# Kernel optimization log

Measured on AMD Instinct MI355X. Metric: run time of the kernel, lower is better.

The kernel has to match this reference:

```python
import jax, jax.numpy as jnp
import numpy as np

EPS = 1e-12
ALPHA = 0.5


def mlp(x, W1, b1, W2, b2):
    # 2-layer MLP (dropout inactive in eval mode) + row-wise l2 norm * 10
    h = jax.nn.relu(x @ W1 + b1)
    y = h @ W2 + b2
    n = jnp.maximum(jnp.linalg.norm(y, axis=-1, keepdims=True), EPS)
    return y / n * 10.0


def setup_inputs() -> dict:
    key = jax.random.key(0)
    ks = jax.random.split(key, 12)
    T, N, F = 3, 100000, 128
    M, E = 4, 65536
    B, H, O = 65536, 128, 64
    X = jax.random.normal(ks[0], (T, N, F), dtype=jnp.float32)
    s_features = jax.random.normal(ks[1], (B, F), dtype=jnp.float32)
    features_map = jax.random.randint(ks[2], (T, N), 0, N)
    s_idxs = jax.random.randint(ks[3], (M, T, E), 0, B)
    t_idxs = jax.random.randint(ks[4], (M, T, E), 0, N)
    weightss = jax.random.uniform(ks[5], (M, T, E), dtype=jnp.float32)
    W1 = jax.random.normal(ks[6], (F, H), dtype=jnp.float32) / np.sqrt(F)
    b1 = jnp.zeros((H,), dtype=jnp.float32)
    W2 = jax.random.normal(ks[7], (H, O), dtype=jnp.float32) / np.sqrt(H)
    b2 = jnp.zeros((O,), dtype=jnp.float32)
    metapath_weights = jnp.ones((M,), dtype=jnp.float32)
    ntype_weights = jnp.ones((T,), dtype=jnp.float32)
    return {"X": X, "s_features": s_features, "features_map": features_map,
            "s_idxs": s_idxs, "t_idxs": t_idxs, "weightss": weightss,
            "batch_size": B, "W1": W1, "b1": b1, "W2": W2, "b2": b2,
            "metapath_weights": metapath_weights, "ntype_weights": ntype_weights}


def reference(X, s_features, features_map, s_idxs, t_idxs, weightss,
              batch_size, W1, b1, W2, b2, metapath_weights, ntype_weights):
    M, T, E = s_idxs.shape
    O = W2.shape[1]
    nm = jax.nn.softmax(metapath_weights)  # [M]
    nt = jax.nn.softmax(ntype_weights)     # [T]
    t_arr = jnp.arange(T)[None, :, None]   # [1,T,1]
    map_idx = features_map[t_arr, t_idxs]  # [M,T,E]
    feats = X[t_arr, map_idx]              # [M,T,E,F] gather
    y = mlp(feats, W1, b1, W2, b2)         # [M,T,E,O]
    # fold metapath & type weights into per-edge weights (scatter is linear)
    ew = weightss * nt[None, :, None] * nm[:, None, None]  # [M,T,E]
    contrib = (y * ew[..., None]).reshape(-1, O)
    seg = s_idxs.reshape(-1)
    out = jax.ops.segment_sum(contrib, seg, num_segments=batch_size)  # [B,O]
    out = (1.0 - ALPHA) * out + ALPHA * mlp(s_features, W1, b1, W2, b2)
    return jax.nn.log_softmax(out, axis=1)
```

## Files before the change

### kernel.cpp

```cpp
#include <hip/hip_runtime.h>

#define Fdim 128
#define Hdim 128
#define Odim 64
#define RT 64
#define ECAP 64
#define EPSV 1e-12f
#define ALPHAV 0.5f

typedef _Float16 h8_t __attribute__((ext_vector_type(8)));
typedef _Float16 h4_t __attribute__((ext_vector_type(4)));
typedef float f32x4 __attribute__((ext_vector_type(4)));

#define X_OFF   0
#define H_OFF   16384
#define LDS_BYTES 32768
#define WIMG_BYTES 49152

extern "C" __global__ __launch_bounds__(512, 4)
void mlp_all(const float* __restrict__ X, const float* __restrict__ S,
             const char* __restrict__ wimg, const float* __restrict__ b1,
             const float* __restrict__ b2,
             _Float16* __restrict__ Yh, float* __restrict__ out,
             int TN, int rows_total)
{
    extern __shared__ char smem[];
    const int tid  = threadIdx.x;
    const int wave = tid >> 6;
    const int lane = tid & 63;
    const int c = lane & 15;
    const int g = lane >> 4;
    const int row0 = blockIdx.x * RT;

    h8_t w1f[4];
    #pragma unroll
    for (int kt = 0; kt < 4; ++kt)
        w1f[kt] = *(const h8_t*)(wimg + (((wave * 4 + kt) * 64 + lane) << 4));

    const int hbase = wave * 16 + 4 * g;
    float b1v[4];
    #pragma unroll
    for (int j = 0; j < 4; ++j) b1v[j] = b1[hbase + j];

    #pragma unroll
    for (int it = 0; it < 4; ++it) {
        int idx = tid + it * 512;
        int r = idx >> 5, c4 = idx & 31;
        int rowg = row0 + r;
        float4 v = make_float4(0.f, 0.f, 0.f, 0.f);
        if (rowg < TN)               v = *(const float4*)(X + (size_t)rowg * Fdim + c4 * 4);
        else if (rowg < rows_total)  v = *(const float4*)(S + (size_t)(rowg - TN) * Fdim + c4 * 4);
        h4_t hv;
        hv[0] = (_Float16)v.x; hv[1] = (_Float16)v.y;
        hv[2] = (_Float16)v.z; hv[3] = (_Float16)v.w;
        *(h4_t*)(smem + X_OFF + ((r * 256 + c4 * 8) ^ ((r & 7) << 4))) = hv;
    }
    __syncthreads();

    f32x4 acc[4];
    #pragma unroll
    for (int r = 0; r < 4; ++r) acc[r] = (f32x4){0.f, 0.f, 0.f, 0.f};

    #pragma unroll
    for (int kt = 0; kt < 4; ++kt) {
        #pragma unroll
        for (int rt = 0; rt < 4; ++rt) {
            int xr = rt * 16 + c;
            h8_t bf = *(const h8_t*)(smem + X_OFF + ((xr * 256 + kt * 64 + g * 16) ^ ((c & 7) << 4)));
            acc[rt] = __builtin_amdgcn_mfma_f32_16x16x32_f16(w1f[kt], bf, acc[rt], 0, 0, 0);
        }
    }

    #pragma unroll
    for (int rt = 0; rt < 4; ++rt) {
        int xr = rt * 16 + c;
        h4_t hv;
        #pragma unroll
        for (int j = 0; j < 4; ++j) {
            float hval = acc[rt][j] + b1v[j];
            hval = fmaxf(hval, 0.f);
            hv[j] = (_Float16)hval;
        }
        *(h4_t*)(smem + H_OFF + ((xr * 256 + hbase * 2) ^ ((xr & 7) << 4))) = hv;
    }
    __syncthreads();

    if (wave < 4) {
        f32x4 acc2[4];
        #pragma unroll
        for (int ct = 0; ct < 4; ++ct) acc2[ct] = (f32x4){0.f, 0.f, 0.f, 0.f};

        #pragma unroll
        for (int kt = 0; kt < 4; ++kt) {
            int xr = wave * 16 + c;
            h8_t a = *(const h8_t*)(smem + H_OFF + ((xr * 256 + kt * 64 + g * 16) ^ ((xr & 7) << 4)));
            #pragma unroll
            for (int ct = 0; ct < 4; ++ct) {
                h8_t bf = *(const h8_t*)(wimg + 32768 + (((ct * 4 + kt) * 64 + lane) << 4));
                acc2[ct] = __builtin_amdgcn_mfma_f32_16x16x32_f16(a, bf, acc2[ct], 0, 0, 0);
            }
        }

        float bb[4];
        #pragma unroll
        for (int ct = 0; ct < 4; ++ct) bb[ct] = b2[ct * 16 + c];

        float y[4][4];
        float ssq[4] = {0.f, 0.f, 0.f, 0.f};
        #pragma unroll
        for (int ct = 0; ct < 4; ++ct) {
            #pragma unroll
            for (int j = 0; j < 4; ++j) {
                float v = acc2[ct][j] + bb[ct];
                y[ct][j] = v;
                ssq[j] += v * v;
            }
        }
        #pragma unroll
        for (int j = 0; j < 4; ++j) {
            float s = ssq[j];
            s += __shfl_xor(s, 1);
            s += __shfl_xor(s, 2);
            s += __shfl_xor(s, 4);
            s += __shfl_xor(s, 8);
            float n  = fmaxf(sqrtf(s), EPSV);
            float sc = 10.0f / n;
            int rowg = row0 + wave * 16 + 4 * g + j;
            if (rowg < TN) {
                _Float16* dst = Yh + (size_t)rowg * Odim;
                #pragma unroll
                for (int ct = 0; ct < 4; ++ct)
                    dst[ct * 16 + c] = (_Float16)(y[ct][j] * sc);
            } else if (rowg < rows_total) {
                float* dst = out + (size_t)(rowg - TN) * Odim;
                #pragma unroll
                for (int ct = 0; ct < 4; ++ct)
                    dst[ct * 16 + c] = ALPHAV * y[ct][j] * sc;
            }
        }
    }
}

extern "C" __global__ __launch_bounds__(256)
void prep_all(const float* __restrict__ W1, const float* __restrict__ W2,
              char* __restrict__ wimg, int* __restrict__ cnt, int B)
{
    if (blockIdx.x < 96) {
        int idx = blockIdx.x * 256 + threadIdx.x;
        if (idx < 16384) {
            int j = idx & 7, l = (idx >> 3) & 63, kt = (idx >> 9) & 3, w = idx >> 11;
            float v = W1[(size_t)(kt * 32 + (l >> 4) * 8 + j) * Hdim + (w * 16 + (l & 15))];
            ((_Float16*)wimg)[idx] = (_Float16)v;
        } else if (idx < 24576) {
            int e2 = idx - 16384;
            int j = e2 & 7, l = (e2 >> 3) & 63, kt = (e2 >> 9) & 3, ct = e2 >> 11;
            float v = W2[(size_t)(kt * 32 + (l >> 4) * 8 + j) * Odim + (ct * 16 + (l & 15))];
            ((_Float16*)(wimg + 32768))[e2] = (_Float16)v;
        }
    } else {
        int i = (blockIdx.x - 96) * 256 + threadIdx.x;
        if (i < B) cnt[i] = 0;
    }
}

extern "C" __global__ __launch_bounds__(256)
void scatter_edges(const int* __restrict__ s_idxs, const int* __restrict__ t_idxs,
                   const float* __restrict__ wss, const int* __restrict__ fmap,
                   const float* __restrict__ mw, const float* __restrict__ tw,
                   int* __restrict__ cnt, int2* __restrict__ edat,
                   int Nn, int Tt, int Mm, int Eslab)
{
    const int slab = blockIdx.y;
    const int t    = slab % Tt;
    const int tN   = t * Nn;
    float mmax = -1e30f, tmax = -1e30f, msum = 0.f, tsum = 0.f;
    for (int i = 0; i < Mm; ++i) mmax = fmaxf(mmax, mw[i]);
    for (int i = 0; i < Mm; ++i) msum += expf(mw[i] - mmax);
    for (int i = 0; i < Tt; ++i) tmax = fmaxf(tmax, tw[i]);
    for (int i = 0; i < Tt; ++i) tsum += expf(tw[i] - tmax);
    const float scale = (1.0f - ALPHAV) * expf(mw[slab / Tt] - mmax) * expf(tw[t] - tmax)
                        / (msum * tsum);

    int i = blockIdx.x * 256 + threadIdx.x;
    if (i >= Eslab) return;
    int e = slab * Eslab + i;
    int si   = s_idxs[e];
    int yrow = tN + fmap[tN + t_idxs[e]];
    float w  = wss[e] * scale;
    int pos = atomicAdd(cnt + si, 1);
    if (pos < ECAP)
        edat[(size_t)si * ECAP + pos] = make_int2(yrow, __float_as_int(w));
}

extern "C" __global__ __launch_bounds__(256)
void row_gather(const int2* __restrict__ edgedat, const int* __restrict__ cnt,
                const _Float16* __restrict__ Yh, float* __restrict__ out, int B)
{
    const int lane = threadIdx.x & 63;
    const int grp8 = lane >> 3;
    const int sub  = lane & 7;
    int b = blockIdx.x * 4 + (threadIdx.x >> 6);
    if (b >= B) return;
    int n = cnt[b];
    if (n > ECAP) n = ECAP;
    const int2* ebase = edgedat + (size_t)b * ECAP;

    float acc[8];
    #pragma unroll
    for (int j = 0; j < 8; ++j) acc[j] = 0.f;

    for (int e = grp8; e < n; e += 8) {
        int2 ed = ebase[e];
        float w = __int_as_float(ed.y);
        h8_t y8 = *(const h8_t*)(Yh + (size_t)ed.x * Odim + sub * 8);
        #pragma unroll
        for (int j = 0; j < 8; ++j) acc[j] += w * (float)y8[j];
    }
    #pragma unroll
    for (int d = 8; d < 64; d <<= 1) {
        #pragma unroll
        for (int j = 0; j < 8; ++j) acc[j] += __shfl_xor(acc[j], d);
    }
    const float* orow = out + (size_t)b * Odim + sub * 8;
    float v[8];
    #pragma unroll
    for (int j = 0; j < 8; ++j) v[j] = orow[j] + acc[j];

    float mx = v[0];
    #pragma unroll
    for (int j = 1; j < 8; ++j) mx = fmaxf(mx, v[j]);
    #pragma unroll
    for (int d = 1; d < 8; d <<= 1) mx = fmaxf(mx, __shfl_xor(mx, d));
    float sm = 0.f;
    #pragma unroll
    for (int j = 0; j < 8; ++j) sm += expf(v[j] - mx);
    #pragma unroll
    for (int d = 1; d < 8; d <<= 1) sm += __shfl_xor(sm, d);
    float lg = mx + logf(sm);

    if (grp8 == 0) {
        float* dst = out + (size_t)b * Odim + sub * 8;
        #pragma unroll
        for (int j = 0; j < 8; ++j) dst[j] = v[j] - lg;
    }
}


extern "C" __global__ __launch_bounds__(256)
void edge_scatter(const int* __restrict__ s_idxs, const int* __restrict__ t_idxs,
                  const float* __restrict__ weightss, const int* __restrict__ fmap,
                  const _Float16* __restrict__ Yh, const float* __restrict__ mw,
                  const float* __restrict__ tw,
                  float* __restrict__ out, int Nn, int Tt, int Mm, int Eslab)
{
    const int lane = threadIdx.x & 63;
    const int slab = blockIdx.y;
    const int t    = slab % Tt;
    const int tN   = t * Nn;
    float mmax = -1e30f, tmax = -1e30f, msum = 0.f, tsum = 0.f;
    for (int i = 0; i < Mm; ++i) mmax = fmaxf(mmax, mw[i]);
    for (int i = 0; i < Mm; ++i) msum += expf(mw[i] - mmax);
    for (int i = 0; i < Tt; ++i) tmax = fmaxf(tmax, tw[i]);
    for (int i = 0; i < Tt; ++i) tsum += expf(tw[i] - tmax);
    const float scale = (1.0f - ALPHAV) * expf(mw[slab / Tt] - mmax) * expf(tw[t] - tmax)
                        / (msum * tsum);

    const int wid  = blockIdx.x * (blockDim.x >> 6) + (threadIdx.x >> 6);
    const int off  = wid * 64;
    if (off >= Eslab) return;

    const int ebase = slab * Eslab + off;
    int   e_ok = (off + lane) < Eslab;
    int   eidx = ebase + (e_ok ? lane : 0);
    int   si   = s_idxs[eidx];
    int   ti   = t_idxs[eidx];
    float w    = e_ok ? (weightss[eidx] * scale) : 0.0f;
    int   yrow = tN + fmap[tN + ti];

    #pragma unroll 8
    for (int i = 0; i < 64; ++i) {
        int   nd = __builtin_amdgcn_readlane(yrow, i);
        int   s  = __builtin_amdgcn_readlane(si, i);
        float ws = __uint_as_float(__builtin_amdgcn_readlane(__float_as_uint(w), i));
        float yv = (float)Yh[(size_t)nd * Odim + lane];
        atomicAdd(out + (size_t)s * Odim + lane, yv * ws);
    }
}

extern "C" __global__ __launch_bounds__(256)
void log_softmax_rows(float* __restrict__ out, int Brows)
{
    int lane = threadIdx.x & 63;
    int r = blockIdx.x * 4 + (threadIdx.x >> 6);
    if (r >= Brows) return;
    float* row = out + (size_t)r * Odim;
    float v = row[lane];
    float mx = v;
    for (int off = 32; off > 0; off >>= 1) mx = fmaxf(mx, __shfl_xor(mx, off));
    float ex = expf(v - mx);
    float s = ex;
    for (int off = 32; off > 0; off >>= 1) s += __shfl_xor(s, off);
    row[lane] = v - mx - logf(s);
}

extern "C" void kernel_launch(void* const* d_in, const int* in_sizes, int n_in,
                              void* d_out, int out_size, void* d_ws, size_t ws_size,
                              hipStream_t stream)
{
    const float* X   = (const float*)d_in[0];
    const float* S   = (const float*)d_in[1];
    const int*   fmap= (const int*)d_in[2];
    const int*   sidx= (const int*)d_in[3];
    const int*   tidx= (const int*)d_in[4];
    const float* wss = (const float*)d_in[5];
    const float* W1  = (const float*)d_in[7];
    const float* b1  = (const float*)d_in[8];
    const float* W2  = (const float*)d_in[9];
    const float* b2  = (const float*)d_in[10];
    const float* mw  = (const float*)d_in[11];
    const float* tw  = (const float*)d_in[12];
    float* out = (float*)d_out;

    const int M = in_sizes[11];
    const int T = in_sizes[12];
    const int H = in_sizes[8];
    const int Fv = in_sizes[7] / H;
    const int N = in_sizes[2] / T;
    const int nedges = in_sizes[3];
    const int E = nedges / (M * T);
    const int B = in_sizes[1] / Fv;
    const int TN = T * N;
    const int rows_total = TN + B;
    const int ngroups = (rows_total + RT - 1) / RT;

    char* wp = (char*)d_ws;
    size_t used = 0;
    auto alloc = [&](size_t bytes) -> char* {
        char* p = wp + used;
        used = (used + bytes + 255) & ~(size_t)255;
        return p;
    };
    _Float16* Yh   = (_Float16*)alloc((size_t)TN * Odim * sizeof(_Float16));
    char*     wimg = (char*)    alloc((size_t)WIMG_BYTES);
    int*      cntp = (int*)     alloc((size_t)B * sizeof(int));
    int2*     edat = (int2*)    alloc((size_t)B * ECAP * sizeof(int2));
    bool bucket_ok = used <= ws_size;

    const int zb = (B + 255) / 256;
    prep_all<<<96 + zb, 256, 0, stream>>>(W1, W2, wimg, cntp, B);

    if (bucket_ok) {
        dim3 sg((E + 255) / 256, M * T);
        scatter_edges<<<sg, 256, 0, stream>>>(sidx, tidx, wss, fmap, mw, tw,
                                              cntp, edat, N, T, M, E);
        mlp_all<<<ngroups, 512, LDS_BYTES, stream>>>(X, S, wimg, b1, b2, Yh, out,
                                                     TN, rows_total);
        row_gather<<<(B + 3) / 4, 256, 0, stream>>>(edat, cntp, Yh, out, B);
    } else {
        mlp_all<<<ngroups, 512, LDS_BYTES, stream>>>(X, S, wimg, b1, b2, Yh, out,
                                                     TN, rows_total);
        int waves_per_slab = (E + 63) / 64;
        dim3 sg((waves_per_slab + 3) / 4, M * T);
        edge_scatter<<<sg, 256, 0, stream>>>(sidx, tidx, wss, fmap, Yh, mw, tw, out,
                                             N, T, M, E);
        log_softmax_rows<<<(B + 3) / 4, 256, 0, stream>>>(out, B);
    }
}
```

Baseline: 148.1 us.

## Split second-layer GEMM across all eight waves with LDS row-norm reduction

The second MLP layer used to run on only four of the eight waves, each computing all 64 output columns. Now every wave computes 16 rows by 32 columns, and W2 fragments are preloaded into registers before the first layer. Per-row partial sums of squares from the two column halves are combined through shared memory behind an extra barrier. This spreads the layer-2 MFMA and epilogue work evenly across waves. The cost is a second __syncthreads and more live registers under launch_bounds(512,4).

```diff
diff --git a/kernel.cpp b/kernel.cpp
--- a/kernel.cpp
+++ b/kernel.cpp
@@ -31,11 +31,19 @@
     const int c = lane & 15;
     const int g = lane >> 4;
     const int row0 = blockIdx.x * RT;
+    const int rw = wave & 3;
+    const int ch = wave >> 2;
 
     h8_t w1f[4];
     #pragma unroll
     for (int kt = 0; kt < 4; ++kt)
         w1f[kt] = *(const h8_t*)(wimg + (((wave * 4 + kt) * 64 + lane) << 4));
+    h8_t w2f[2][4];
+    #pragma unroll
+    for (int c2 = 0; c2 < 2; ++c2)
+        #pragma unroll
+        for (int kt = 0; kt < 4; ++kt)
+            w2f[c2][kt] = *(const h8_t*)(wimg + 32768 + ((((ch * 2 + c2) * 4 + kt) * 64 + lane) << 4));
 
     const int hbase = wave * 16 + 4 * g;
     float b1v[4];
@@ -85,58 +93,68 @@
     }
     __syncthreads();
 
-    if (wave < 4) {
-        f32x4 acc2[4];
-        #pragma unroll
-        for (int ct = 0; ct < 4; ++ct) acc2[ct] = (f32x4){0.f, 0.f, 0.f, 0.f};
-
-        #pragma unroll
-        for (int kt = 0; kt < 4; ++kt) {
-            int xr = wave * 16 + c;
-            h8_t a = *(const h8_t*)(smem + H_OFF + ((xr * 256 + kt * 64 + g * 16) ^ ((xr & 7) << 4)));
+    f32x4 acc2[2];
+    #pragma unroll
+    for (int c2 = 0; c2 < 2; ++c2) acc2[c2] = (f32x4){0.f, 0.f, 0.f, 0.f};
+
+    #pragma unroll
+    for (int kt = 0; kt < 4; ++kt) {
+        int xr = rw * 16 + c;
+        h8_t a = *(const h8_t*)(smem + H_OFF + ((xr * 256 + kt * 64 + g * 16) ^ ((xr & 7) << 4)));
+        #pragma unroll
+        for (int c2 = 0; c2 < 2; ++c2)
+            acc2[c2] = __builtin_amdgcn_mfma_f32_16x16x32_f16(a, w2f[c2][kt], acc2[c2], 0, 0, 0);
+    }
+
+    float bb[2];
+    #pragma unroll
+    for (int c2 = 0; c2 < 2; ++c2) bb[c2] = b2[(ch * 2 + c2) * 16 + c];
+
+    float y[2][4];
+    float ssq[4] = {0.f, 0.f, 0.f, 0.f};
+    #pragma unroll
+    for (int c2 = 0; c2 < 2; ++c2) {
+        #pragma unroll
+        for (int j = 0; j < 4; ++j) {
+            float v = acc2[c2][j] + bb[c2];
+            y[c2][j] = v;
+            ssq[j] += v * v;
+        }
+    }
+    #pragma unroll
+    for (int j = 0; j < 4; ++j) {
+        float s = ssq[j];
+        s += __shfl_xor(s, 1);
+        s += __shfl_xor(s, 2);
+        s += __shfl_xor(s, 4);
+        s += __shfl_xor(s, 8);
+        ssq[j] = s;
+    }
+    float* arr = (float*)(smem + X_OFF);
+    if (c == 0) {
+        #pragma unroll
+        for (int j = 0; j < 4; ++j)
+            arr[ch * 64 + rw * 16 + 4 * g + j] = ssq[j];
+    }
+    __syncthreads();
+
+    #pragma unroll
+    for (int j = 0; j < 4; ++j) {
+        int row = rw * 16 + 4 * g + j;
+        float tot = arr[row] + arr[64 + row];
+        float n  = fmaxf(sqrtf(tot), EPSV);
+        float sc = 10.0f / n;
+        int rowg = row0 + row;
+        if (rowg < TN) {
+            _Float16* dst = Yh + (size_t)rowg * Odim;
             #pragma unroll
-            for (int ct = 0; ct < 4; ++ct) {
-                h8_t bf = *(const h8_t*)(wimg + 32768 + (((ct * 4 + kt) * 64 + lane) << 4));
-                acc2[ct] = __builtin_amdgcn_mfma_f32_16x16x32_f16(a, bf, acc2[ct], 0, 0, 0);
-            }
-        }
-
-        float bb[4];
-        #pragma unroll
-        for (int ct = 0; ct < 4; ++ct) bb[ct] = b2[ct * 16 + c];
-
-        float y[4][4];
-        float ssq[4] = {0.f, 0.f, 0.f, 0.f};
-        #pragma unroll
-        for (int ct = 0; ct < 4; ++ct) {
+            for (int c2 = 0; c2 < 2; ++c2)
+                dst[(ch * 2 + c2) * 16 + c] = (_Float16)(y[c2][j] * sc);
+        } else if (rowg < rows_total) {
+            float* dst = out + (size_t)(rowg - TN) * Odim;
             #pragma unroll
-            for (int j = 0; j < 4; ++j) {
-                float v = acc2[ct][j] + bb[ct];
-                y[ct][j] = v;
-                ssq[j] += v * v;
-            }
-        }
-        #pragma unroll
-        for (int j = 0; j < 4; ++j) {
-            float s = ssq[j];
-            s += __shfl_xor(s, 1);
-            s += __shfl_xor(s, 2);
-            s += __shfl_xor(s, 4);
-            s += __shfl_xor(s, 8);
-            float n  = fmaxf(sqrtf(s), EPSV);
-            float sc = 10.0f / n;
-            int rowg = row0 + wave * 16 + 4 * g + j;
-            if (rowg < TN) {
-                _Float16* dst = Yh + (size_t)rowg * Odim;
-                #pragma unroll
-                for (int ct = 0; ct < 4; ++ct)
-                    dst[ct * 16 + c] = (_Float16)(y[ct][j] * sc);
-            } else if (rowg < rows_total) {
-                float* dst = out + (size_t)(rowg - TN) * Odim;
-                #pragma unroll
-                for (int ct = 0; ct < 4; ++ct)
-                    dst[ct * 16 + c] = ALPHAV * y[ct][j] * sc;
-            }
+            for (int c2 = 0; c2 < 2; ++c2)
+                dst[(ch * 2 + c2) * 16 + c] = ALPHAV * y[c2][j] * sc;
         }
     }
 }
```

New measurement: 164.9 us. +11.3%, slower.
